# Optimization experiments

Hardware: AMD Instinct MI355X
Metric: run time of the kernel (lower is better)

The kernel has to match this reference:

```python
import jax, jax.numpy as jnp
import numpy as np

B, N, D_IN = 8, 1369, 768
S, D, ITERS = 7, 256, 3
RES, SIGMA = 37, 5.0
EPS = 1e-8


def _ln(x, g, b):
    m = jnp.mean(x, -1, keepdims=True)
    v = jnp.mean((x - m) ** 2, -1, keepdims=True)
    return (x - m) * jax.lax.rsqrt(v + 1e-5) * g + b


def _abs_grid():
    xs = jnp.linspace(-1.0, 1.0, RES)
    ys = jnp.linspace(-1.0, 1.0, RES)
    gx, gy = jnp.meshgrid(xs, ys, indexing='xy')
    return jnp.stack([gx.reshape(-1), gy.reshape(-1)], axis=-1)  # [N,2]


def setup_inputs() -> dict:
    key = jax.random.key(0)
    ks = jax.random.split(key, 40)
    i = iter(range(40))
    def w(shape, scale=0.02):
        return (jax.random.normal(ks[next(i)], shape, jnp.float32) * scale).astype(jnp.float32)
    def zeros(shape):
        return jnp.zeros(shape, jnp.float32)
    xav = float(np.sqrt(6.0 / (S + D)))
    inp = {
        'inputs': jax.random.normal(ks[next(i)], (B, N, D_IN), jnp.float32),
        'slots_init_p': jax.random.uniform(ks[next(i)], (1, S, D), jnp.float32, -xav, xav),
        'S_s0': w((1, S, 1, 2)),
        'S_p0': w((1, S, 1, 2)),
        'im_ln1_g': jnp.ones((D_IN,), jnp.float32), 'im_ln1_b': zeros((D_IN,)),
        'im_w1': w((D_IN, D_IN)), 'im_b1': zeros((D_IN,)),
        'im_w2': w((D_IN, D)), 'im_b2': zeros((D,)),
        'im_ln2_g': jnp.ones((D,), jnp.float32), 'im_ln2_b': zeros((D,)),
        'Wq': w((D, D)), 'Wk': w((D, D)), 'Wv': w((D, D)),
        'g_w': w((2, D)), 'g_b': zeros((D,)),
        'f_w1': w((D, D)), 'f_b1': zeros((D,)),
        'f_w2': w((D, D)), 'f_b2': zeros((D,)),
        'ln_g': jnp.ones((D,), jnp.float32), 'ln_b': zeros((D,)),
        'gru_wih': w((D, 3 * D)), 'gru_whh': w((D, 3 * D)),
        'gru_bih': zeros((3 * D,)), 'gru_bhh': zeros((3 * D,)),
        'mlp_ln_g': jnp.ones((D,), jnp.float32), 'mlp_ln_b': zeros((D,)),
        'mlp_w1': w((D, 4 * D)), 'mlp_b1': zeros((4 * D,)),
        'mlp_w2': w((4 * D, D)), 'mlp_b2': zeros((D,)),
        'fin_w': w((D, D)), 'fin_b': zeros((D,)),
    }
    return inp


def reference(inputs, slots_init_p, S_s0, S_p0,
              im_ln1_g, im_ln1_b, im_w1, im_b1, im_w2, im_b2, im_ln2_g, im_ln2_b,
              Wq, Wk, Wv, g_w, g_b, f_w1, f_b1, f_w2, f_b2,
              ln_g, ln_b, gru_wih, gru_whh, gru_bih, gru_bhh,
              mlp_ln_g, mlp_ln_b, mlp_w1, mlp_b1, mlp_w2, mlp_b2,
              fin_w, fin_b):
    abs_grid = _abs_grid()                    # [N,2], constant buffer
    ag = abs_grid[None, None]                 # [1,1,N,2]
    scale = D ** (-0.5)

    slots = jnp.broadcast_to(slots_init_p, (B, S, D))
    slots_init = slots

    # initial_mlp: LN -> Linear -> ReLU -> Linear -> LN (dropout-free eval path)
    x = _ln(inputs, im_ln1_g, im_ln1_b)
    x = jax.nn.relu(x @ im_w1 + im_b1)
    x = x @ im_w2 + im_b2
    x = _ln(x, im_ln2_g, im_ln2_b)            # [B,N,D]
    KX = x @ Wk                                # slot-independent part of K(inputs)
    VX = x @ Wv

    S_p = jnp.broadcast_to(S_p0, (B, S, 1, 2))
    S_s = jnp.broadcast_to(S_s0, (B, S, 1, 2))

    def f_mlp(z):
        return jax.nn.relu(z @ f_w1 + f_b1) @ f_w2 + f_b2

    attn = None
    slots_prev = slots
    for t in range(ITERS + 1):
        if t == ITERS - 1:  # query_opt straight-through trick
            slots = jax.lax.stop_gradient(slots) + slots_init - jax.lax.stop_gradient(slots_init)
        slots_prev = slots
        sn = _ln(slots, ln_g, ln_b)
        rel = (ag - S_p) / (S_s * SIGMA)      # [B,S,N,2]
        grel = rel @ g_w + g_b                # [B,S,N,D]
        k = f_mlp(KX[:, None] + grel)         # [B,S,N,D]
        v = f_mlp(VX[:, None] + grel)
        q = sn @ Wq                           # [B,S,D]
        dots = jnp.einsum('bsd,bsnd->bsn', q, k) * scale
        attn = jax.nn.softmax(dots, axis=1) + EPS   # softmax over slots
        attn = attn / jnp.sum(attn, -1, keepdims=True)
        updates = jnp.einsum('bsnd,bsn->bsd', v, attn)
        S_p = jnp.einsum('bsn,nd->bsd', attn, abs_grid)[:, :, None, :]
        S_s = jnp.sqrt(jnp.einsum('bsnd,bsn->bsd', (ag - S_p) ** 2, attn))[:, :, None, :]
        if t != ITERS:
            # GRUCell (torch gate order r,z,n)
            gi = updates @ gru_wih + gru_bih
            gh = slots_prev @ gru_whh + gru_bhh
            i_r, i_z, i_n = jnp.split(gi, 3, axis=-1)
            h_r, h_z, h_n = jnp.split(gh, 3, axis=-1)
            r = jax.nn.sigmoid(i_r + h_r)
            z = jax.nn.sigmoid(i_z + h_z)
            n = jnp.tanh(i_n + r * h_n)
            slots = (1.0 - z) * n + z * slots_prev
            # residual pre-norm MLP (dropout identity in eval)
            m = _ln(slots, mlp_ln_g, mlp_ln_b)
            m = jax.nn.relu(m @ mlp_w1 + mlp_b1) @ mlp_w2 + mlp_b2
            slots = slots + m
    out = slots_prev @ fin_w + fin_b
    return out, attn
```

## Files before the change

kernel.cpp:

```cpp
#include <hip/hip_runtime.h>

constexpr int CB   = 8;
constexpr int CN   = 1369;
constexpr int CDIN = 768;
constexpr int CS   = 7;
constexpr int CD   = 256;
constexpr int CITERS = 3;
constexpr int CRES = 37;
constexpr float CSIGMA = 5.0f;
constexpr int CBS = CB * CS;
constexpr int CBN = CB * CN;
constexpr int CKV = 2 * CD;
constexpr float LNEPS = 1e-5f;
constexpr float ATTN_EPS = 1e-8f;

typedef unsigned short u16;
typedef short bs8 __attribute__((ext_vector_type(8)));
typedef float f4 __attribute__((ext_vector_type(4)));

__device__ __forceinline__ float ag_x(int n) { return -1.f + (float)(n % CRES) * (2.f / 36.f); }
__device__ __forceinline__ float ag_y(int n) { return -1.f + (float)(n / CRES) * (2.f / 36.f); }

__device__ __forceinline__ u16 bf_rne(float f) {
    unsigned u = __float_as_uint(f);
    return (u16)((u + 0x7FFFu + ((u >> 16) & 1u)) >> 16);
}
__device__ __forceinline__ float bf_to_f(u16 h) { return __uint_as_float(((unsigned)h) << 16); }

__device__ __forceinline__ void split2b(float v, u16& h, u16& m) {
    h = bf_rne(v);
    m = bf_rne(v - bf_to_f(h));
}

__device__ __forceinline__ void async16(const u16* g, u16* l) {
    __builtin_amdgcn_global_load_lds(
        (const __attribute__((address_space(1))) unsigned int*)g,
        (__attribute__((address_space(3))) unsigned int*)l, 16, 0, 0);
}

__device__ __forceinline__ float block_reduce_sum(float v, float* sbuf) {
    #pragma unroll
    for (int off = 32; off > 0; off >>= 1) v += __shfl_down(v, off, 64);
    if ((threadIdx.x & 63) == 0) sbuf[threadIdx.x >> 6] = v;
    __syncthreads();
    if (threadIdx.x == 0) sbuf[0] = sbuf[0] + sbuf[1] + sbuf[2] + sbuf[3];
    __syncthreads();
    float r = sbuf[0];
    __syncthreads();
    return r;
}

__global__ __launch_bounds__(256) void ln_planes_kernel(const float* __restrict__ in,
        u16* __restrict__ Yh, u16* __restrict__ Ym,
        const float* __restrict__ g, const float* __restrict__ b, int d) {
    __shared__ float sbuf[8];
    int row = blockIdx.x, t = threadIdx.x;
    const float* x = in + (size_t)row * d;
    float v0 = x[t], v1 = 0.f, v2 = 0.f;
    if (d > 256) { v1 = x[t + 256]; v2 = x[t + 512]; }
    float mean = block_reduce_sum(v0 + v1 + v2, sbuf) / d;
    float d0 = v0 - mean, d1 = v1 - mean, d2 = v2 - mean;
    float pv = (d > 256) ? (d0 * d0 + d1 * d1 + d2 * d2) : (d0 * d0);
    float var = block_reduce_sum(pv, sbuf) / d;
    float rstd = rsqrtf(var + LNEPS);
    {
        float y = d0 * rstd * g[t] + b[t];
        u16 h, m; split2b(y, h, m);
        Yh[(size_t)row * d + t] = h; Ym[(size_t)row * d + t] = m;
    }
    if (d > 256) {
        float y1 = d1 * rstd * g[t + 256] + b[t + 256];
        u16 h, m; split2b(y1, h, m);
        Yh[(size_t)row * d + t + 256] = h; Ym[(size_t)row * d + t + 256] = m;
        float y2 = d2 * rstd * g[t + 512] + b[t + 512];
        split2b(y2, h, m);
        Yh[(size_t)row * d + t + 512] = h; Ym[(size_t)row * d + t + 512] = m;
    }
}

__global__ __launch_bounds__(256) void transpose_split2_kernel(const float* __restrict__ W,
        u16* __restrict__ Th, u16* __restrict__ Tm, int K, int N) {
    __shared__ float tile[32][33];
    int nb = blockIdx.x * 32, kb = blockIdx.y * 32;
    int tx = threadIdx.x & 31, ty = threadIdx.x >> 5;
    #pragma unroll
    for (int i = 0; i < 32; i += 8)
        tile[ty + i][tx] = W[(size_t)(kb + ty + i) * N + nb + tx];
    __syncthreads();
    #pragma unroll
    for (int i = 0; i < 32; i += 8) {
        float v = tile[tx][ty + i];
        u16 h, m; split2b(v, h, m);
        size_t idx = (size_t)(nb + ty + i) * K + kb + tx;
        Th[idx] = h; Tm[idx] = m;
    }
}

__global__ __launch_bounds__(256) void wprodT_kernel(const float* __restrict__ A,
        const float* __restrict__ B, u16* __restrict__ Th, u16* __restrict__ Tm) {
    __shared__ float arow[CD];
    int k = blockIdx.x;
    arow[threadIdx.x] = A[k * CD + threadIdx.x];
    __syncthreads();
    int n = threadIdx.x;
    float acc = 0.f;
    for (int j = 0; j < CD; j++) acc += arow[j] * B[(size_t)j * CD + n];
    u16 h, m; split2b(acc, h, m);
    Th[(size_t)n * CD + k] = h;
    Tm[(size_t)n * CD + k] = m;
}

__global__ __launch_bounds__(256) void wprodPq_kernel(const float* __restrict__ Wq,
        const float* __restrict__ f_w2, float* __restrict__ Pq) {
    __shared__ float arow[CD];
    int k = blockIdx.x;
    arow[threadIdx.x] = Wq[k * CD + threadIdx.x];
    __syncthreads();
    int n = threadIdx.x;
    float acc = 0.f;
    for (int c = 0; c < CD; c++) acc += arow[c] * f_w2[(size_t)n * CD + c];
    Pq[(size_t)k * CD + n] = acc;
}

__global__ __launch_bounds__(256) void wprodN_kernel(const float* __restrict__ A,
        const float* __restrict__ B, float* __restrict__ P, int N) {
    __shared__ float arow[CD];
    int k = blockIdx.x;
    arow[threadIdx.x] = A[k * CD + threadIdx.x];
    __syncthreads();
    int n = blockIdx.y * 256 + threadIdx.x;
    if (n >= N) return;
    float acc = 0.f;
    for (int j = 0; j < CD; j++) acc += arow[j] * B[(size_t)j * N + n];
    P[(size_t)k * N + n] = acc;
}

__global__ __launch_bounds__(256) void prep_small_kernel(
        const float* __restrict__ g_w, const float* __restrict__ g_b,
        const float* __restrict__ f_w1, const float* __restrict__ f_b1,
        float* __restrict__ G2, float* __restrict__ gb1,
        const float* __restrict__ f_b2, const float* __restrict__ wih,
        const float* __restrict__ bih, float* __restrict__ bg,
        const float* __restrict__ Wq, float* __restrict__ wqb) {
    int bid = blockIdx.x;
    if (bid == 0) {
        int n = threadIdx.x;
        float a0 = 0.f, a1 = 0.f, ab = 0.f;
        for (int j = 0; j < CD; j++) {
            float w = f_w1[j * CD + n];
            a0 += g_w[j] * w;
            a1 += g_w[CD + j] * w;
            ab += g_b[j] * w;
        }
        G2[n] = a0; G2[CD + n] = a1; gb1[n] = ab + f_b1[n];
    } else if (bid <= 3) {
        int n = (bid - 1) * 256 + threadIdx.x;
        float s = bih[n];
        for (int c = 0; c < CD; c++) s += f_b2[c] * wih[(size_t)c * (3 * CD) + n];
        bg[n] = s;
    } else {
        int j = threadIdx.x;
        float s = 0.f;
        for (int c = 0; c < CD; c++) s += Wq[j * CD + c] * f_b2[c];
        wqb[j] = s;
    }
}

template<int BN>
__global__ __launch_bounds__(256)
void hgemm2(const u16* __restrict__ Ah, const u16* __restrict__ Am,
            const u16* __restrict__ Bh, const u16* __restrict__ Bm,
            int M, int N, int K, const float* __restrict__ bias, int relu,
            float* __restrict__ Cf, u16* __restrict__ Ch, u16* __restrict__ Cm) {
    constexpr int BP = BN * 32;
    constexpr int SB = 4096 + 2 * BP;
    constexpr int NI = 2 + 2 * (BN / 64);
    constexpr int NF = BN / 32;
    constexpr int PP = BN / 64;
    __shared__ u16 smem[3][SB];
    const int tid = threadIdx.x;

    int bx = blockIdx.x, by = blockIdx.y;
    {
        int gx = gridDim.x;
        int nwg = gx * gridDim.y;
        if (!(nwg & 7)) {
            int bid = by * gx + bx;
            int cpx = nwg >> 3;
            int s = (bid & 7) * cpx + (bid >> 3);
            bx = s % gx; by = s / gx;
        }
    }
    const int m0 = by * 64, n0 = bx * BN;
    const int w = tid >> 6, lane = tid & 63;
    const int wm = w & 1, wn = w >> 1;
    const int l15 = lane & 15, l4 = lane >> 4;

    const u16* srcp[NI];
    int dsto[NI];
    #pragma unroll
    for (int i = 0; i < NI; i++) {
        const u16* bp; int row, r, c;
        if (i < 2) {
            int qq = tid;
            r = qq >> 2;
            c = (qq & 3) ^ ((r ^ (r >> 2)) & 3);
            bp = (i == 0) ? Ah : Am;
            row = m0 + r; row = row < M ? row : M - 1;
            dsto[i] = i * 2048 + w * 512;
        } else {
            int ii = i - 2;
            int plane = ii / PP;
            int sub = ii % PP;
            int qq = sub * 256 + tid;
            r = qq >> 2;
            c = (qq & 3) ^ ((r ^ (r >> 2)) & 3);
            bp = plane ? Bm : Bh;
            row = n0 + r;
            dsto[i] = 4096 + plane * BP + sub * 2048 + w * 512;
        }
        srcp[i] = bp + (size_t)row * K + c * 8;
    }

    f4 acc[2][NF];
    #pragma unroll
    for (int i = 0; i < 2; i++)
        #pragma unroll
        for (int j = 0; j < NF; j++) acc[i][j] = (f4){0.f, 0.f, 0.f, 0.f};

    const int cx8 = (l4 ^ (l15 & 3) ^ ((l15 >> 2) & 3)) * 8;

    const int ns = K / 32;
    #pragma unroll
    for (int i = 0; i < NI; i++) async16(srcp[i], &smem[0][dsto[i]]);
    #pragma unroll
    for (int i = 0; i < NI; i++) async16(srcp[i] + 32, &smem[1][dsto[i]]);

    u16* c0 = &smem[0][0];
    u16* c1 = &smem[1][0];
    u16* c2 = &smem[2][0];

    for (int k = 0; k < ns; k++) {
        if (k + 2 < ns) {
            #pragma unroll
            for (int i = 0; i < NI; i++) async16(srcp[i] + (k + 2) * 32, c2 + dsto[i]);
            if constexpr (BN == 128)
                asm volatile("s_waitcnt vmcnt(12)" ::: "memory");
            else
                asm volatile("s_waitcnt vmcnt(8)" ::: "memory");
        } else if (k + 1 < ns) {
            if constexpr (BN == 128)
                asm volatile("s_waitcnt vmcnt(6)" ::: "memory");
            else
                asm volatile("s_waitcnt vmcnt(4)" ::: "memory");
        } else {
            asm volatile("s_waitcnt vmcnt(0)" ::: "memory");
        }
        __builtin_amdgcn_s_barrier();
        bs8 ah[2], am[2], bh[NF], bm[NF];
        #pragma unroll
        for (int f = 0; f < 2; f++) {
            int oa = (wm * 32 + f * 16 + l15) * 32 + cx8;
            ah[f] = *(const bs8*)(c0 + oa);
            am[f] = *(const bs8*)(c0 + 2048 + oa);
        }
        #pragma unroll
        for (int f = 0; f < NF; f++) {
            int ob = (wn * (NF * 16) + f * 16 + l15) * 32 + cx8;
            bh[f] = *(const bs8*)(c0 + 4096 + ob);
            bm[f] = *(const bs8*)(c0 + 4096 + BP + ob);
        }
        #pragma unroll
        for (int mf = 0; mf < 2; mf++)
            #pragma unroll
            for (int nf = 0; nf < NF; nf++) {
                acc[mf][nf] = __builtin_amdgcn_mfma_f32_16x16x32_bf16(am[mf], bh[nf], acc[mf][nf], 0, 0, 0);
                acc[mf][nf] = __builtin_amdgcn_mfma_f32_16x16x32_bf16(ah[mf], bm[nf], acc[mf][nf], 0, 0, 0);
                acc[mf][nf] = __builtin_amdgcn_mfma_f32_16x16x32_bf16(ah[mf], bh[nf], acc[mf][nf], 0, 0, 0);
            }
        asm volatile("" ::: "memory");
        __builtin_amdgcn_s_barrier();
        u16* t_ = c0; c0 = c1; c1 = c2; c2 = t_;
    }

    #pragma unroll
    for (int mf = 0; mf < 2; mf++)
        #pragma unroll
        for (int i = 0; i < 4; i++) {
            int grow = m0 + wm * 32 + mf * 16 + l4 * 4 + i;
            if (grow < M) {
                #pragma unroll
                for (int nf = 0; nf < NF; nf++) {
                    int col = n0 + wn * (NF * 16) + nf * 16 + l15;
                    float v = acc[mf][nf][i] + (bias ? bias[col] : 0.f);
                    if (relu) v = fmaxf(v, 0.f);
                    if (Cf) Cf[(size_t)grow * N + col] = v;
                    else {
                        u16 h, m; split2b(v, h, m);
                        Ch[(size_t)grow * N + col] = h;
                        Cm[(size_t)grow * N + col] = m;
                    }
                }
            }
        }
}

__global__ __launch_bounds__(128) void rowgemm_kernel(const float* __restrict__ A,
        const float* __restrict__ W, const float* __restrict__ bias,
        float* __restrict__ C, int N, int K, int relu,
        const float* __restrict__ resid, const float* __restrict__ resb) {
    __shared__ float sA[1024];
    int r = blockIdx.x;
    int c = blockIdx.y * 128 + threadIdx.x;
    for (int i = threadIdx.x; i < K; i += 128) sA[i] = A[(size_t)r * K + i];
    __syncthreads();
    float a0 = 0.f, a1 = 0.f, a2 = 0.f, a3 = 0.f;
    #pragma unroll 4
    for (int k = 0; k < K; k += 4) {
        a0 += sA[k]     * W[(size_t)k * N + c];
        a1 += sA[k + 1] * W[(size_t)(k + 1) * N + c];
        a2 += sA[k + 2] * W[(size_t)(k + 2) * N + c];
        a3 += sA[k + 3] * W[(size_t)(k + 3) * N + c];
    }
    float v = (a0 + a1) + (a2 + a3) + (bias ? bias[c] : 0.f);
    if (relu) v = fmaxf(v, 0.f);
    if (resid) v += resid[(size_t)r * N + c] + resb[c];
    C[(size_t)r * N + c] = v;
}

__global__ __launch_bounds__(128) void rowgemmG_kernel(
        const float* __restrict__ A0, const float* __restrict__ W0,
        const float* __restrict__ b0, float* __restrict__ C0,
        const float* __restrict__ A1, const float* __restrict__ W1,
        const float* __restrict__ b1, float* __restrict__ C1,
        const float* __restrict__ sc0, int N, int K) {
    __shared__ float sA[256];
    const float* A = blockIdx.z ? A1 : A0;
    const float* W = blockIdx.z ? W1 : W0;
    const float* B = blockIdx.z ? b1 : b0;
    float* C = blockIdx.z ? C1 : C0;
    int r = blockIdx.x;
    int c = blockIdx.y * 128 + threadIdx.x;
    float scl = blockIdx.z ? 1.f : sc0[r];
    for (int i = threadIdx.x; i < K; i += 128) sA[i] = A[(size_t)r * K + i] * scl;
    __syncthreads();
    float a0 = 0.f, a1 = 0.f, a2 = 0.f, a3 = 0.f;
    #pragma unroll 4
    for (int k = 0; k < K; k += 4) {
        a0 += sA[k]     * W[(size_t)k * N + c];
        a1 += sA[k + 1] * W[(size_t)(k + 1) * N + c];
        a2 += sA[k + 2] * W[(size_t)(k + 2) * N + c];
        a3 += sA[k + 3] * W[(size_t)(k + 3) * N + c];
    }
    C[(size_t)r * N + c] = (a0 + a1) + (a2 + a3) + B[c];
}

__global__ __launch_bounds__(256) void init_kernel(const float* __restrict__ slots_init_p,
        const float* __restrict__ S_s0, const float* __restrict__ S_p0,
        float* __restrict__ slots, float* __restrict__ S_s, float* __restrict__ S_p) {
    int bs = blockIdx.x, t = threadIdx.x;
    int s = bs % CS;
    slots[bs * CD + t] = slots_init_p[s * CD + t];
    if (t < 2) { S_s[bs * 2 + t] = S_s0[s * 2 + t]; S_p[bs * 2 + t] = S_p0[s * 2 + t]; }
}

__global__ __launch_bounds__(256) void ln_slots_q_kernel(const float* __restrict__ slots,
        const float* __restrict__ ln_g, const float* __restrict__ ln_b,
        const float* __restrict__ wqb, const float* __restrict__ Pq,
        float* __restrict__ qwb, float* __restrict__ qb0) {
    __shared__ float sbuf[8];
    __shared__ float sN[CD];
    int row = blockIdx.x, t = threadIdx.x;
    float x = slots[row * CD + t];
    float mean = block_reduce_sum(x, sbuf) / CD;
    float d0 = x - mean;
    float var = block_reduce_sum(d0 * d0, sbuf) / CD;
    float sn = d0 * rsqrtf(var + LNEPS) * ln_g[t] + ln_b[t];
    sN[t] = sn;
    float qb = block_reduce_sum(sn * wqb[t], sbuf);
    if (t == 0) qb0[row] = qb;
    __syncthreads();
    float acc = 0.f;
    #pragma unroll 4
    for (int k = 0; k < CD; k++) acc += sN[k] * Pq[(size_t)k * CD + t];
    qwb[row * CD + t] = acc;
}

__global__ __launch_bounds__(256) void dotsv_kernel(const float* __restrict__ KVX,
        const float* __restrict__ S_p, const float* __restrict__ S_s,
        const float* __restrict__ G2, const float* __restrict__ gb1,
        const float* __restrict__ qw, const float* __restrict__ qb0,
        float* __restrict__ attn, float* __restrict__ Wacc) {
    __shared__ float sred[4 * CD];
    int b = blockIdx.x;
    int w = threadIdx.x >> 6, l = threadIdx.x & 63;
    int k4 = l * 4;
    float4 g0 = *(const float4*)(G2 + k4);
    float4 g1 = *(const float4*)(G2 + CD + k4);
    float4 gb = *(const float4*)(gb1 + k4);
    float4 qwv[CS]; float px[CS], py[CS], ix[CS], iy[CS], q0[CS];
    #pragma unroll
    for (int s = 0; s < CS; s++) {
        int bs = b * CS + s;
        qwv[s] = *(const float4*)(qw + bs * CD + k4);
        px[s] = S_p[2 * bs]; py[s] = S_p[2 * bs + 1];
        ix[s] = 1.f / (S_s[2 * bs] * CSIGMA); iy[s] = 1.f / (S_s[2 * bs + 1] * CSIGMA);
        q0[s] = qb0[bs];
    }
    float4 acc[CS];
    #pragma unroll
    for (int s = 0; s < CS; s++) acc[s] = make_float4(0.f, 0.f, 0.f, 0.f);
    int nbase = blockIdx.y * 16 + w * 4;
    #pragma unroll
    for (int i = 0; i < 4; i++) {
        int n = nbase + i;
        int nc = n < CN ? n : CN - 1;
        const float* rowp = KVX + (size_t)(b * CN + nc) * CKV;
        float4 kx = *(const float4*)(rowp + k4);
        float ax = ag_x(nc), ay = ag_y(nc);
        float dsv[CS];
        #pragma unroll
        for (int s = 0; s < CS; s++) {
            float r0 = (ax - px[s]) * ix[s];
            float r1 = (ay - py[s]) * iy[s];
            float v0 = fmaxf(kx.x + r0 * g0.x + r1 * g1.x + gb.x, 0.f);
            float v1 = fmaxf(kx.y + r0 * g0.y + r1 * g1.y + gb.y, 0.f);
            float v2 = fmaxf(kx.z + r0 * g0.z + r1 * g1.z + gb.z, 0.f);
            float v3 = fmaxf(kx.w + r0 * g0.w + r1 * g1.w + gb.w, 0.f);
            float d = v0 * qwv[s].x + v1 * qwv[s].y + v2 * qwv[s].z + v3 * qwv[s].w;
            #pragma unroll
            for (int off = 32; off > 0; off >>= 1) d += __shfl_xor(d, off, 64);
            dsv[s] = 0.0625f * (d + q0[s]);
        }
        float mx = -1e30f;
        #pragma unroll
        for (int s = 0; s < CS; s++) mx = fmaxf(mx, dsv[s]);
        float sum = 0.f;
        #pragma unroll
        for (int s = 0; s < CS; s++) { dsv[s] = __expf(dsv[s] - mx); sum += dsv[s]; }
        float inv = 1.f / sum;
        #pragma unroll
        for (int s = 0; s < CS; s++) dsv[s] = dsv[s] * inv + ATTN_EPS;
        if (l == 0 && n < CN) {
            #pragma unroll
            for (int s = 0; s < CS; s++)
                attn[(size_t)(b * CS + s) * CN + n] = dsv[s];
        }
        if (Wacc && n < CN) {
            float4 vx = *(const float4*)(rowp + CD + k4);
            #pragma unroll
            for (int s = 0; s < CS; s++) {
                float r0 = (ax - px[s]) * ix[s];
                float r1 = (ay - py[s]) * iy[s];
                float a = dsv[s];
                acc[s].x += a * fmaxf(vx.x + r0 * g0.x + r1 * g1.x + gb.x, 0.f);
                acc[s].y += a * fmaxf(vx.y + r0 * g0.y + r1 * g1.y + gb.y, 0.f);
                acc[s].z += a * fmaxf(vx.z + r0 * g0.z + r1 * g1.z + gb.z, 0.f);
                acc[s].w += a * fmaxf(vx.w + r0 * g0.w + r1 * g1.w + gb.w, 0.f);
            }
        }
    }
    if (Wacc) {
        for (int s = 0; s < CS; s++) {
            ((float4*)sred)[w * 64 + l] = acc[s];
            __syncthreads();
            if (threadIdx.x < CD) {
                float v = sred[threadIdx.x] + sred[CD + threadIdx.x]
                        + sred[2 * CD + threadIdx.x] + sred[3 * CD + threadIdx.x];
                atomicAdd(&Wacc[(size_t)(b * CS + s) * CD + threadIdx.x], v);
            }
            __syncthreads();
        }
    }
}

__global__ __launch_bounds__(256) void attn_moments_kernel(float* __restrict__ u,
        float* __restrict__ S_p, float* __restrict__ S_s, float* __restrict__ inv0,
        int writeNorm) {
    __shared__ float sbuf[8];
    int bs = blockIdx.x;
    float* up = u + (size_t)bs * CN;
    float m0 = 0, m1x = 0, m1y = 0, m2x = 0, m2y = 0;
    for (int n = threadIdx.x; n < CN; n += 256) {
        float uu = up[n];
        float ax = ag_x(n), ay = ag_y(n);
        m0 += uu; m1x += uu * ax; m1y += uu * ay; m2x += uu * ax * ax; m2y += uu * ay * ay;
    }
    m0  = block_reduce_sum(m0, sbuf);
    m1x = block_reduce_sum(m1x, sbuf);
    m1y = block_reduce_sum(m1y, sbuf);
    m2x = block_reduce_sum(m2x, sbuf);
    m2y = block_reduce_sum(m2y, sbuf);
    float px = m1x / m0, py = m1y / m0;
    float inv = 1.f / m0;
    if (threadIdx.x == 0) {
        S_p[2 * bs] = px; S_p[2 * bs + 1] = py;
        S_s[2 * bs]     = sqrtf(fmaxf(m2x / m0 - px * px, 0.f));
        S_s[2 * bs + 1] = sqrtf(fmaxf(m2y / m0 - py * py, 0.f));
        inv0[bs] = inv;
    }
    if (writeNorm)
        for (int n = threadIdx.x; n < CN; n += 256) up[n] = up[n] * inv;
}

__global__ __launch_bounds__(256) void gate_ln_kernel(const float* __restrict__ giRaw,
        const float* __restrict__ ghRaw, const float* __restrict__ slots,
        const float* __restrict__ mg, const float* __restrict__ mb,
        float* __restrict__ snewb, float* __restrict__ sMb) {
    __shared__ float sbuf[8];
    int row = blockIdx.x, t = threadIdx.x;
    float gi0 = giRaw[row * 3 * CD + t];
    float gi1 = giRaw[row * 3 * CD + CD + t];
    float gi2 = giRaw[row * 3 * CD + 2 * CD + t];
    float gh0 = ghRaw[row * 3 * CD + t];
    float gh1 = ghRaw[row * 3 * CD + CD + t];
    float gh2 = ghRaw[row * 3 * CD + 2 * CD + t];
    float r = 1.f / (1.f + expf(-(gi0 + gh0)));
    float z = 1.f / (1.f + expf(-(gi1 + gh1)));
    float nn = tanhf(gi2 + r * gh2);
    float snew = (1.f - z) * nn + z * slots[row * CD + t];
    snewb[row * CD + t] = snew;
    float mean = block_reduce_sum(snew, sbuf) / CD;
    float dv = snew - mean;
    float var = block_reduce_sum(dv * dv, sbuf) / CD;
    sMb[row * CD + t] = dv * rsqrtf(var + LNEPS) * mg[t] + mb[t];
}

extern "C" void kernel_launch(void* const* d_in, const int* in_sizes, int n_in,
                              void* d_out, int out_size, void* d_ws, size_t ws_size,
                              hipStream_t stream) {
    (void)in_sizes; (void)n_in; (void)out_size;
    const float* inputs       = (const float*)d_in[0];
    const float* slots_init_p = (const float*)d_in[1];
    const float* S_s0         = (const float*)d_in[2];
    const float* S_p0         = (const float*)d_in[3];
    const float* im_ln1_g = (const float*)d_in[4];
    const float* im_ln1_b = (const float*)d_in[5];
    const float* im_w1    = (const float*)d_in[6];
    const float* im_b1    = (const float*)d_in[7];
    const float* im_w2    = (const float*)d_in[8];
    const float* im_b2    = (const float*)d_in[9];
    const float* im_ln2_g = (const float*)d_in[10];
    const float* im_ln2_b = (const float*)d_in[11];
    const float* Wq  = (const float*)d_in[12];
    const float* Wk  = (const float*)d_in[13];
    const float* Wv  = (const float*)d_in[14];
    const float* g_w = (const float*)d_in[15];
    const float* g_b = (const float*)d_in[16];
    const float* f_w1 = (const float*)d_in[17];
    const float* f_b1 = (const float*)d_in[18];
    const float* f_w2 = (const float*)d_in[19];
    const float* f_b2 = (const float*)d_in[20];
    const float* ln_g = (const float*)d_in[21];
    const float* ln_b = (const float*)d_in[22];
    const float* gru_wih = (const float*)d_in[23];
    const float* gru_whh = (const float*)d_in[24];
    const float* gru_bih = (const float*)d_in[25];
    const float* gru_bhh = (const float*)d_in[26];
    const float* mlp_ln_g = (const float*)d_in[27];
    const float* mlp_ln_b = (const float*)d_in[28];
    const float* mlp_w1 = (const float*)d_in[29];
    const float* mlp_b1 = (const float*)d_in[30];
    const float* mlp_w2 = (const float*)d_in[31];
    const float* mlp_b2 = (const float*)d_in[32];
    const float* fin_w = (const float*)d_in[33];
    const float* fin_b = (const float*)d_in[34];

    char* base = (char*)d_ws;
    size_t off = 0;
    auto take = [&](size_t bytes) { void* p = base + off; off += (bytes + 255) & ~(size_t)255; return p; };

    float* R1 = (float*)take((size_t)CBN * CDIN * 4);
    float* R2 = (float*)take((size_t)CBN * CDIN * 4);
    u16* w1th = (u16*)take((size_t)CDIN * CDIN * 2);
    u16* w1tm = (u16*)take((size_t)CDIN * CDIN * 2);
    u16* w2th = (u16*)take((size_t)CDIN * CD * 2);
    u16* w2tm = (u16*)take((size_t)CDIN * CD * 2);
    u16* kvth = (u16*)take((size_t)CKV * CD * 2);
    u16* kvtm = (u16*)take((size_t)CKV * CD * 2);
    float* G2b  = (float*)take((size_t)2 * CD * 4);
    float* gb1b = (float*)take((size_t)CD * 4);
    float* Pq   = (float*)take((size_t)CD * CD * 4);
    float* Pg   = (float*)take((size_t)CD * 3 * CD * 4);
    float* bgv  = (float*)take((size_t)3 * CD * 4);
    float* wqbb = (float*)take((size_t)CD * 4);
    float* qwb   = (float*)take((size_t)CBS * CD * 4);
    float* qb0b  = (float*)take((size_t)CBS * 4);
    float* inv0b = (float*)take((size_t)CBS * 4);
    float* Wacc  = (float*)take((size_t)CBS * CD * 4);
    float* giRaw = (float*)take((size_t)CBS * 3 * CD * 4);
    float* ghRaw = (float*)take((size_t)CBS * 3 * CD * 4);
    float* snewb = (float*)take((size_t)CBS * CD * 4);
    float* sMb   = (float*)take((size_t)CBS * CD * 4);
    float* h1b   = (float*)take((size_t)CBS * 4 * CD * 4);
    float* S_pA  = (float*)take((size_t)CBS * 2 * 4);
    float* S_sA  = (float*)take((size_t)CBS * 2 * 4);
    float* S_pB  = (float*)take((size_t)CBS * 2 * 4);
    float* S_sB  = (float*)take((size_t)CBS * 2 * 4);
    float* slots = (float*)take((size_t)CBS * CD * 4);
    if (ws_size < off) return;

    u16* xlnh = (u16*)R1;
    u16* xlnm = xlnh + (size_t)CBN * CDIN;
    u16* X1h  = (u16*)R2;
    u16* X1m  = X1h + (size_t)CBN * CDIN;
    float* xD = R1;
    u16* xDnh = (u16*)(R1 + (size_t)CBN * CD);
    u16* xDnm = xDnh + (size_t)CBN * CD;
    float* KVX = R2;

    float* out0 = (float*)d_out;
    float* attnb = out0 + CBS * CD;

    dim3 blk(256);
    const int gM = (CBN + 63) / 64;
    dim3 gridBN(CB, 86);

    transpose_split2_kernel<<<dim3(CDIN/32, CDIN/32), blk, 0, stream>>>(im_w1, w1th, w1tm, CDIN, CDIN);
    transpose_split2_kernel<<<dim3(CD/32,   CDIN/32), blk, 0, stream>>>(im_w2, w2th, w2tm, CDIN, CD);
    wprodT_kernel<<<dim3(CD), blk, 0, stream>>>(Wk, f_w1, kvth, kvtm);
    wprodT_kernel<<<dim3(CD), blk, 0, stream>>>(Wv, f_w1,
        kvth + (size_t)CD * CD, kvtm + (size_t)CD * CD);
    wprodPq_kernel<<<dim3(CD), blk, 0, stream>>>(Wq, f_w2, Pq);
    wprodN_kernel<<<dim3(CD, 3), blk, 0, stream>>>(f_w2, gru_wih, Pg, 3 * CD);
    prep_small_kernel<<<dim3(5), blk, 0, stream>>>(g_w, g_b, f_w1, f_b1, G2b, gb1b,
        f_b2, gru_wih, gru_bih, bgv, Wq, wqbb);

    ln_planes_kernel<<<CBN, blk, 0, stream>>>(inputs, xlnh, xlnm, im_ln1_g, im_ln1_b, CDIN);
    hgemm2<64><<<dim3(CDIN/64, gM), blk, 0, stream>>>(xlnh, xlnm, w1th, w1tm,
        CBN, CDIN, CDIN, im_b1, 1, nullptr, X1h, X1m);
    hgemm2<64><<<dim3(CD/64, gM), blk, 0, stream>>>(X1h, X1m, w2th, w2tm,
        CBN, CD, CDIN, im_b2, 0, xD, nullptr, nullptr);
    ln_planes_kernel<<<CBN, blk, 0, stream>>>(xD, xDnh, xDnm, im_ln2_g, im_ln2_b, CD);
    hgemm2<64><<<dim3(CKV/64, gM), blk, 0, stream>>>(xDnh, xDnm, kvth, kvtm,
        CBN, CKV, CD, nullptr, 0, KVX, nullptr, nullptr);
    init_kernel<<<CBS, blk, 0, stream>>>(slots_init_p, S_s0, S_p0, slots, S_sA, S_pA);

    for (int t = 0; t <= CITERS; t++) {
        float* Sp_cur = (t & 1) ? S_pB : S_pA;
        float* Ss_cur = (t & 1) ? S_sB : S_sA;
        float* Sp_nxt = (t & 1) ? S_pA : S_pB;
        float* Ss_nxt = (t & 1) ? S_sA : S_sB;
        ln_slots_q_kernel<<<CBS, blk, 0, stream>>>(slots, ln_g, ln_b, wqbb, Pq, qwb, qb0b);
        if (t < CITERS) {
            hipMemsetAsync(Wacc, 0, (size_t)CBS * CD * sizeof(float), stream);
            dotsv_kernel<<<gridBN, blk, 0, stream>>>(KVX, Sp_cur, Ss_cur, G2b, gb1b,
                qwb, qb0b, attnb, Wacc);
        } else {
            dotsv_kernel<<<gridBN, blk, 0, stream>>>(KVX, Sp_cur, Ss_cur, G2b, gb1b,
                qwb, qb0b, attnb, nullptr);
        }
        attn_moments_kernel<<<CBS, blk, 0, stream>>>(attnb, Sp_nxt, Ss_nxt, inv0b,
            t == CITERS ? 1 : 0);
        if (t < CITERS) {
            rowgemmG_kernel<<<dim3(CBS, 3*CD/128, 2), dim3(128), 0, stream>>>(
                Wacc, Pg, bgv, giRaw, slots, gru_whh, gru_bhh, ghRaw, inv0b, 3 * CD, CD);
            gate_ln_kernel<<<CBS, blk, 0, stream>>>(giRaw, ghRaw, slots,
                mlp_ln_g, mlp_ln_b, snewb, sMb);
            rowgemm_kernel<<<dim3(CBS, 4*CD/128), dim3(128), 0, stream>>>(sMb, mlp_w1, mlp_b1,
                h1b, 4 * CD, CD, 1, nullptr, nullptr);
            rowgemm_kernel<<<dim3(CBS, CD/128), dim3(128), 0, stream>>>(h1b, mlp_w2, nullptr,
                slots, CD, 4 * CD, 0, snewb, mlp_b2);
        }
    }
    rowgemm_kernel<<<dim3(CBS, CD/128), dim3(128), 0, stream>>>(slots, fin_w, fin_b,
        out0, CD, CD, 0, nullptr, nullptr);
}
```

Before: 661.4 us.

## Fuse attention moment sums into dotsv and retune first GEMM tile/buffering

The dotsv kernel now accumulates per-slot attention moments (sum, first and second moments of grid coords) and atomically adds them into a small buffer. Next-iteration position/scale and the GRU update normalization are derived from that buffer, so the intermediate attn_moments kernel and its attention-map write are skipped except in the final iteration. Zeroing of Wacc and the moment buffers moves into gate_ln, which drops a per-iteration memset. The first image-MLP GEMM switches to a 128-wide tile with double buffering, adding an NBUF template parameter. The trade-off is float atomics and E[x^2]-E[x]^2 variance, which are less numerically stable than the two-pass form.

```diff
diff --git a/kernel.cpp b/kernel.cpp
--- a/kernel.cpp
+++ b/kernel.cpp
@@ -166,7 +166,7 @@
     }
 }
 
-template<int BN>
+template<int BN, int NBUF>
 __global__ __launch_bounds__(256)
 void hgemm2(const u16* __restrict__ Ah, const u16* __restrict__ Am,
             const u16* __restrict__ Bh, const u16* __restrict__ Bm,
@@ -177,7 +177,7 @@
     constexpr int NI = 2 + 2 * (BN / 64);
     constexpr int NF = BN / 32;
     constexpr int PP = BN / 64;
-    __shared__ u16 smem[3][SB];
+    __shared__ u16 smem[NBUF][SB];
     const int tid = threadIdx.x;
 
     int bx = blockIdx.x, by = blockIdx.y;
@@ -232,29 +232,36 @@
 
     const int ns = K / 32;
     #pragma unroll
-    for (int i = 0; i < NI; i++) async16(srcp[i], &smem[0][dsto[i]]);
-    #pragma unroll
-    for (int i = 0; i < NI; i++) async16(srcp[i] + 32, &smem[1][dsto[i]]);
+    for (int d = 0; d < NBUF - 1; d++)
+        #pragma unroll
+        for (int i = 0; i < NI; i++) async16(srcp[i] + d * 32, &smem[d][dsto[i]]);
 
     u16* c0 = &smem[0][0];
-    u16* c1 = &smem[1][0];
-    u16* c2 = &smem[2][0];
+    u16* c1 = &smem[NBUF > 1 ? 1 : 0][0];
+    u16* c2 = &smem[NBUF - 1][0];
 
     for (int k = 0; k < ns; k++) {
-        if (k + 2 < ns) {
-            #pragma unroll
-            for (int i = 0; i < NI; i++) async16(srcp[i] + (k + 2) * 32, c2 + dsto[i]);
-            if constexpr (BN == 128)
-                asm volatile("s_waitcnt vmcnt(12)" ::: "memory");
-            else
-                asm volatile("s_waitcnt vmcnt(8)" ::: "memory");
-        } else if (k + 1 < ns) {
-            if constexpr (BN == 128)
-                asm volatile("s_waitcnt vmcnt(6)" ::: "memory");
-            else
-                asm volatile("s_waitcnt vmcnt(4)" ::: "memory");
+        if constexpr (NBUF == 3) {
+            if (k + 2 < ns) {
+                #pragma unroll
+                for (int i = 0; i < NI; i++) async16(srcp[i] + (k + 2) * 32, c2 + dsto[i]);
+                if constexpr (BN == 64) asm volatile("s_waitcnt vmcnt(8)" ::: "memory");
+                else                     asm volatile("s_waitcnt vmcnt(12)" ::: "memory");
+            } else if (k + 1 < ns) {
+                if constexpr (BN == 64) asm volatile("s_waitcnt vmcnt(4)" ::: "memory");
+                else                     asm volatile("s_waitcnt vmcnt(6)" ::: "memory");
+            } else {
+                asm volatile("s_waitcnt vmcnt(0)" ::: "memory");
+            }
         } else {
-            asm volatile("s_waitcnt vmcnt(0)" ::: "memory");
+            if (k + 1 < ns) {
+                #pragma unroll
+                for (int i = 0; i < NI; i++) async16(srcp[i] + (k + 1) * 32, c1 + dsto[i]);
+                if constexpr (BN == 64) asm volatile("s_waitcnt vmcnt(4)" ::: "memory");
+                else                     asm volatile("s_waitcnt vmcnt(6)" ::: "memory");
+            } else {
+                asm volatile("s_waitcnt vmcnt(0)" ::: "memory");
+            }
         }
         __builtin_amdgcn_s_barrier();
         bs8 ah[2], am[2], bh[NF], bm[NF];
@@ -280,7 +287,8 @@
             }
         asm volatile("" ::: "memory");
         __builtin_amdgcn_s_barrier();
-        u16* t_ = c0; c0 = c1; c1 = c2; c2 = t_;
+        if constexpr (NBUF == 3) { u16* t_ = c0; c0 = c1; c1 = c2; c2 = t_; }
+        else                     { u16* t_ = c0; c0 = c1; c1 = t_; }
     }
 
     #pragma unroll
@@ -333,7 +341,7 @@
         const float* __restrict__ b0, float* __restrict__ C0,
         const float* __restrict__ A1, const float* __restrict__ W1,
         const float* __restrict__ b1, float* __restrict__ C1,
-        const float* __restrict__ sc0, int N, int K) {
+        const float* __restrict__ msum, int N, int K) {
     __shared__ float sA[256];
     const float* A = blockIdx.z ? A1 : A0;
     const float* W = blockIdx.z ? W1 : W0;
@@ -341,7 +349,7 @@
     float* C = blockIdx.z ? C1 : C0;
     int r = blockIdx.x;
     int c = blockIdx.y * 128 + threadIdx.x;
-    float scl = blockIdx.z ? 1.f : sc0[r];
+    float scl = blockIdx.z ? 1.f : 1.f / msum[r * 8];
     for (int i = threadIdx.x; i < K; i += 128) sA[i] = A[(size_t)r * K + i] * scl;
     __syncthreads();
     float a0 = 0.f, a1 = 0.f, a2 = 0.f, a3 = 0.f;
@@ -388,9 +396,11 @@
 
 __global__ __launch_bounds__(256) void dotsv_kernel(const float* __restrict__ KVX,
         const float* __restrict__ S_p, const float* __restrict__ S_s,
+        const float* __restrict__ msum_in, int useMsum,
         const float* __restrict__ G2, const float* __restrict__ gb1,
         const float* __restrict__ qw, const float* __restrict__ qb0,
-        float* __restrict__ attn, float* __restrict__ Wacc) {
+        float* __restrict__ attn, float* __restrict__ Wacc,
+        float* __restrict__ msum_out) {
     __shared__ float sred[4 * CD];
     int b = blockIdx.x;
     int w = threadIdx.x >> 6, l = threadIdx.x & 63;
@@ -403,13 +413,26 @@
     for (int s = 0; s < CS; s++) {
         int bs = b * CS + s;
         qwv[s] = *(const float4*)(qw + bs * CD + k4);
-        px[s] = S_p[2 * bs]; py[s] = S_p[2 * bs + 1];
-        ix[s] = 1.f / (S_s[2 * bs] * CSIGMA); iy[s] = 1.f / (S_s[2 * bs + 1] * CSIGMA);
+        if (useMsum) {
+            const float* mp = msum_in + bs * 8;
+            float m0 = mp[0];
+            float pxv = mp[1] / m0, pyv = mp[2] / m0;
+            float sx = sqrtf(fmaxf(mp[3] / m0 - pxv * pxv, 0.f));
+            float sy = sqrtf(fmaxf(mp[4] / m0 - pyv * pyv, 0.f));
+            px[s] = pxv; py[s] = pyv;
+            ix[s] = 1.f / (sx * CSIGMA); iy[s] = 1.f / (sy * CSIGMA);
+        } else {
+            px[s] = S_p[2 * bs]; py[s] = S_p[2 * bs + 1];
+            ix[s] = 1.f / (S_s[2 * bs] * CSIGMA); iy[s] = 1.f / (S_s[2 * bs + 1] * CSIGMA);
+        }
         q0[s] = qb0[bs];
     }
     float4 acc[CS];
     #pragma unroll
     for (int s = 0; s < CS; s++) acc[s] = make_float4(0.f, 0.f, 0.f, 0.f);
+    float wm0[CS], wm1x[CS], wm1y[CS], wm2x[CS], wm2y[CS];
+    #pragma unroll
+    for (int s = 0; s < CS; s++) { wm0[s] = 0.f; wm1x[s] = 0.f; wm1y[s] = 0.f; wm2x[s] = 0.f; wm2y[s] = 0.f; }
     int nbase = blockIdx.y * 16 + w * 4;
     #pragma unroll
     for (int i = 0; i < 4; i++) {
@@ -441,10 +464,19 @@
         float inv = 1.f / sum;
         #pragma unroll
         for (int s = 0; s < CS; s++) dsv[s] = dsv[s] * inv + ATTN_EPS;
-        if (l == 0 && n < CN) {
+        if (attn && l == 0 && n < CN) {
             #pragma unroll
             for (int s = 0; s < CS; s++)
                 attn[(size_t)(b * CS + s) * CN + n] = dsv[s];
+        }
+        if (msum_out && n < CN) {
+            float ax2 = ax * ax, ay2 = ay * ay;
+            #pragma unroll
+            for (int s = 0; s < CS; s++) {
+                float a = dsv[s];
+                wm0[s] += a; wm1x[s] += a * ax; wm1y[s] += a * ay;
+                wm2x[s] += a * ax2; wm2y[s] += a * ay2;
+            }
         }
         if (Wacc && n < CN) {
             float4 vx = *(const float4*)(rowp + CD + k4);
@@ -472,6 +504,25 @@
             __syncthreads();
         }
     }
+    if (msum_out) {
+        if (l == 0) {
+            #pragma unroll
+            for (int s = 0; s < CS; s++) {
+                sred[w * 40 + s * 5 + 0] = wm0[s];
+                sred[w * 40 + s * 5 + 1] = wm1x[s];
+                sred[w * 40 + s * 5 + 2] = wm1y[s];
+                sred[w * 40 + s * 5 + 3] = wm2x[s];
+                sred[w * 40 + s * 5 + 4] = wm2y[s];
+            }
+        }
+        __syncthreads();
+        if (threadIdx.x < 35) {
+            int s = threadIdx.x / 5, j = threadIdx.x % 5;
+            float v = sred[s * 5 + j] + sred[40 + s * 5 + j]
+                    + sred[80 + s * 5 + j] + sred[120 + s * 5 + j];
+            atomicAdd(&msum_out[(size_t)(b * CS + s) * 8 + j], v);
+        }
+    }
 }
 
 __global__ __launch_bounds__(256) void attn_moments_kernel(float* __restrict__ u,
@@ -506,7 +557,8 @@
 __global__ __launch_bounds__(256) void gate_ln_kernel(const float* __restrict__ giRaw,
         const float* __restrict__ ghRaw, const float* __restrict__ slots,
         const float* __restrict__ mg, const float* __restrict__ mb,
-        float* __restrict__ snewb, float* __restrict__ sMb) {
+        float* __restrict__ snewb, float* __restrict__ sMb,
+        float* __restrict__ WaccZ, float* __restrict__ msumZ) {
     __shared__ float sbuf[8];
     int row = blockIdx.x, t = threadIdx.x;
     float gi0 = giRaw[row * 3 * CD + t];
@@ -520,6 +572,8 @@
     float nn = tanhf(gi2 + r * gh2);
     float snew = (1.f - z) * nn + z * slots[row * CD + t];
     snewb[row * CD + t] = snew;
+    WaccZ[row * CD + t] = 0.f;
+    if (t < 8) msumZ[row * 8 + t] = 0.f;
     float mean = block_reduce_sum(snew, sbuf) / CD;
     float dv = snew - mean;
     float var = block_reduce_sum(dv * dv, sbuf) / CD;
@@ -587,7 +641,9 @@
     float* qwb   = (float*)take((size_t)CBS * CD * 4);
     float* qb0b  = (float*)take((size_t)CBS * 4);
     float* inv0b = (float*)take((size_t)CBS * 4);
-    float* Wacc  = (float*)take((size_t)CBS * CD * 4);
+    float* Wacc  = (float*)take(((size_t)CBS * CD + 2 * CBS * 8) * 4);
+    float* msumA = Wacc + (size_t)CBS * CD;
+    float* msumB = msumA + (size_t)CBS * 8;
     float* giRaw = (float*)take((size_t)CBS * 3 * CD * 4);
     float* ghRaw = (float*)take((size_t)CBS * 3 * CD * 4);
     float* snewb = (float*)take((size_t)CBS * CD * 4);
@@ -600,6 +656,8 @@
     float* slots = (float*)take((size_t)CBS * CD * 4);
     if (ws_size < off) return;
 
+    float* msum[2] = {msumA, msumB};
+
     u16* xlnh = (u16*)R1;
     u16* xlnm = xlnh + (size_t)CBN * CDIN;
     u16* X1h  = (u16*)R2;
@@ -625,42 +683,37 @@
     wprodN_kernel<<<dim3(CD, 3), blk, 0, stream>>>(f_w2, gru_wih, Pg, 3 * CD);
     prep_small_kernel<<<dim3(5), blk, 0, stream>>>(g_w, g_b, f_w1, f_b1, G2b, gb1b,
         f_b2, gru_wih, gru_bih, bgv, Wq, wqbb);
+    hipMemsetAsync(Wacc, 0, ((size_t)CBS * CD + 2 * CBS * 8) * sizeof(float), stream);
 
     ln_planes_kernel<<<CBN, blk, 0, stream>>>(inputs, xlnh, xlnm, im_ln1_g, im_ln1_b, CDIN);
-    hgemm2<64><<<dim3(CDIN/64, gM), blk, 0, stream>>>(xlnh, xlnm, w1th, w1tm,
+    hgemm2<128,2><<<dim3(CDIN/128, gM), blk, 0, stream>>>(xlnh, xlnm, w1th, w1tm,
         CBN, CDIN, CDIN, im_b1, 1, nullptr, X1h, X1m);
-    hgemm2<64><<<dim3(CD/64, gM), blk, 0, stream>>>(X1h, X1m, w2th, w2tm,
+    hgemm2<64,3><<<dim3(CD/64, gM), blk, 0, stream>>>(X1h, X1m, w2th, w2tm,
         CBN, CD, CDIN, im_b2, 0, xD, nullptr, nullptr);
     ln_planes_kernel<<<CBN, blk, 0, stream>>>(xD, xDnh, xDnm, im_ln2_g, im_ln2_b, CD);
-    hgemm2<64><<<dim3(CKV/64, gM), blk, 0, stream>>>(xDnh, xDnm, kvth, kvtm,
+    hgemm2<64,3><<<dim3(CKV/64, gM), blk, 0, stream>>>(xDnh, xDnm, kvth, kvtm,
         CBN, CKV, CD, nullptr, 0, KVX, nullptr, nullptr);
     init_kernel<<<CBS, blk, 0, stream>>>(slots_init_p, S_s0, S_p0, slots, S_sA, S_pA);
 
     for (int t = 0; t <= CITERS; t++) {
-        float* Sp_cur = (t & 1) ? S_pB : S_pA;
-        float* Ss_cur = (t & 1) ? S_sB : S_sA;
-        float* Sp_nxt = (t & 1) ? S_pA : S_pB;
-        float* Ss_nxt = (t & 1) ? S_sA : S_sB;
         ln_slots_q_kernel<<<CBS, blk, 0, stream>>>(slots, ln_g, ln_b, wqbb, Pq, qwb, qb0b);
         if (t < CITERS) {
-            hipMemsetAsync(Wacc, 0, (size_t)CBS * CD * sizeof(float), stream);
-            dotsv_kernel<<<gridBN, blk, 0, stream>>>(KVX, Sp_cur, Ss_cur, G2b, gb1b,
-                qwb, qb0b, attnb, Wacc);
-        } else {
-            dotsv_kernel<<<gridBN, blk, 0, stream>>>(KVX, Sp_cur, Ss_cur, G2b, gb1b,
-                qwb, qb0b, attnb, nullptr);
-        }
-        attn_moments_kernel<<<CBS, blk, 0, stream>>>(attnb, Sp_nxt, Ss_nxt, inv0b,
-            t == CITERS ? 1 : 0);
-        if (t < CITERS) {
+            dotsv_kernel<<<gridBN, blk, 0, stream>>>(KVX, S_pA, S_sA,
+                msum[(t + 1) & 1], t > 0 ? 1 : 0, G2b, gb1b,
+                qwb, qb0b, nullptr, Wacc, msum[t & 1]);
             rowgemmG_kernel<<<dim3(CBS, 3*CD/128, 2), dim3(128), 0, stream>>>(
-                Wacc, Pg, bgv, giRaw, slots, gru_whh, gru_bhh, ghRaw, inv0b, 3 * CD, CD);
+                Wacc, Pg, bgv, giRaw, slots, gru_whh, gru_bhh, ghRaw, msum[t & 1], 3 * CD, CD);
             gate_ln_kernel<<<CBS, blk, 0, stream>>>(giRaw, ghRaw, slots,
-                mlp_ln_g, mlp_ln_b, snewb, sMb);
+                mlp_ln_g, mlp_ln_b, snewb, sMb, Wacc, msum[(t + 1) & 1]);
             rowgemm_kernel<<<dim3(CBS, 4*CD/128), dim3(128), 0, stream>>>(sMb, mlp_w1, mlp_b1,
                 h1b, 4 * CD, CD, 1, nullptr, nullptr);
             rowgemm_kernel<<<dim3(CBS, CD/128), dim3(128), 0, stream>>>(h1b, mlp_w2, nullptr,
                 slots, CD, 4 * CD, 0, snewb, mlp_b2);
+        } else {
+            dotsv_kernel<<<gridBN, blk, 0, stream>>>(KVX, S_pA, S_sA,
+                msum[(t + 1) & 1], 1, G2b, gb1b,
+                qwb, qb0b, attnb, nullptr, nullptr);
+            attn_moments_kernel<<<CBS, blk, 0, stream>>>(attnb, S_pB, S_sB, inv0b, 1);
         }
     }
     rowgemm_kernel<<<dim3(CBS, CD/128), dim3(128), 0, stream>>>(slots, fin_w, fin_b,
```

Result: no change. 665.6 us (+0.6%).
